# Performance work log

Measured on AMD Instinct MI355X. Metric: run time of the kernel, lower is better.

## Reference

```python
import jax, jax.numpy as jnp
import numpy as np

B, T, D, H = 4, 2048, 1024, 16
HD = D // H  # head_dim = 64

def setup_inputs() -> dict:
    key = jax.random.key(0)
    k1, k2, k3 = jax.random.split(key, 3)
    x = jax.random.normal(k1, (B, T, D), dtype=jnp.float32)
    w_qkv = jax.random.normal(k2, (D, 3 * D), dtype=jnp.float32) * (D ** -0.5)
    b_qkv = jnp.zeros((3 * D,), dtype=jnp.float32)
    w_proj = jax.random.normal(k3, (D, D), dtype=jnp.float32) * (D ** -0.5)
    b_proj = jnp.zeros((D,), dtype=jnp.float32)
    return {"x": x, "w_qkv": w_qkv, "b_qkv": b_qkv, "w_proj": w_proj, "b_proj": b_proj}

def reference(x, w_qkv, b_qkv, w_proj, b_proj):
    b, t, d = x.shape
    scale = HD ** -0.5
    qkv = x @ w_qkv + b_qkv                          # [B,T,3D]
    qkv = qkv.reshape(b, t, 3, H, HD)
    qkv = jnp.transpose(qkv, (2, 0, 3, 1, 4))        # [3,B,H,T,HD]
    q, k, v = qkv[0], qkv[1], qkv[2]
    att = jnp.einsum("bhqd,bhkd->bhqk", q, k) * scale  # [B,H,T,T]
    mask = jnp.tril(jnp.ones((t, t), dtype=att.dtype))[None, None]
    att = att * mask + (1.0 - mask) * (-1e9)
    att = jax.nn.softmax(att, axis=-1)
    # dropout inactive (training=False)
    y = jnp.einsum("bhqk,bhkd->bhqd", att, v)        # [B,H,T,HD]
    y = jnp.transpose(y, (0, 2, 1, 3)).reshape(b, t, d)
    return y @ w_proj + b_proj
```

## Files before the change

kernel.cpp:

```cpp
#include <hip/hip_runtime.h>
#include <hip/hip_bf16.h>

typedef unsigned short u16;
typedef short short8 __attribute__((ext_vector_type(8)));
typedef short bf16x4 __attribute__((ext_vector_type(4)));
typedef float f32x4 __attribute__((ext_vector_type(4)));
typedef float f32x16 __attribute__((ext_vector_type(16)));

#define B_SZ 4
#define T_SEQ 2048
#define DMODEL 1024
#define NH 16
#define HD 64
#define QKV_ELEMS 8388608ull
#define QSCALE (0.125f * 1.44269504f)

__device__ __forceinline__ u16 f2bf(float f) {
    __hip_bfloat16 h = __float2bfloat16(f);
    return __builtin_bit_cast(u16, h);
}

__device__ __forceinline__ void gload16(const void* g, void* l) {
    __builtin_amdgcn_global_load_lds(
        (const __attribute__((address_space(1))) unsigned int*)g,
        (__attribute__((address_space(3))) unsigned int*)l, 16, 0, 0);
}

#define NCX 2048
__global__ __launch_bounds__(256) void prep_kernel(
    const float4* __restrict__ x, u16* __restrict__ xb,
    const float* __restrict__ w_qkv, u16* __restrict__ wqT,
    const float* __restrict__ w_proj, u16* __restrict__ wpT)
{
    const int b = blockIdx.x;
    if (b < NCX) {
        int i = b * 256 + threadIdx.x;
#pragma unroll
        for (int rep = 0; rep < 4; ++rep, i += NCX * 256) {
            const float4 v = x[i];
            union { u16 u[4]; uint2 d; } p;
            p.u[0] = f2bf(v.x); p.u[1] = f2bf(v.y);
            p.u[2] = f2bf(v.z); p.u[3] = f2bf(v.w);
            *(uint2*)(xb + (size_t)i * 4) = p.d;
        }
    } else if (b < NCX + 192) {
        const int bb2 = b - NCX;
        const int n = (bb2 % 12) * 256 + threadIdx.x;
        const int k0 = (bb2 / 12) * 64;
        for (int kk = 0; kk < 64; kk += 8) {
            short8 o;
#pragma unroll
            for (int e = 0; e < 8; ++e)
                o[e] = (short)f2bf(w_qkv[(size_t)(k0 + kk + e) * 3072 + n]);
            *(short8*)&wqT[(size_t)n * 1024 + k0 + kk] = o;
        }
    } else {
        const int bb2 = b - NCX - 192;
        const int n = (bb2 % 4) * 256 + threadIdx.x;
        const int k0 = (bb2 / 4) * 64;
        for (int kk = 0; kk < 64; kk += 8) {
            short8 o;
#pragma unroll
            for (int e = 0; e < 8; ++e)
                o[e] = (short)f2bf(w_proj[(size_t)(k0 + kk + e) * 1024 + n]);
            *(short8*)&wpT[(size_t)n * 1024 + k0 + kk] = o;
        }
    }
}

template <int EPI>
__global__ __launch_bounds__(256) void gemm_kernel(
    const u16* __restrict__ A, const u16* __restrict__ Bt,
    const float* __restrict__ bias, void* __restrict__ outp)
{
    __shared__ u16 As[128 * 64];
    __shared__ u16 Bs[128 * 64];
    const int tid = threadIdx.x;
    const int l = tid & 63;
    const int w = tid >> 6;
    const int wm = w >> 1, wn = w & 1;
    const int m0 = blockIdx.y * 128, n0 = blockIdx.x * 128;
    const int srow = l >> 3;
    const int sch  = (l & 7) ^ srow;
    const int fr = l & 15, fq = l >> 4;

    f32x4 acc[4][4] = {};

    for (int k0 = 0; k0 < 1024; k0 += 64) {
        __syncthreads();
#pragma unroll
        for (int ii = 0; ii < 4; ++ii) {
            const int row = w * 32 + ii * 8;
            gload16(&A[(size_t)(m0 + row + srow) * 1024 + k0 + sch * 8], &As[row * 64]);
            gload16(&Bt[(size_t)(n0 + row + srow) * 1024 + k0 + sch * 8], &Bs[row * 64]);
        }
        __syncthreads();
#pragma unroll
        for (int ks = 0; ks < 2; ++ks) {
            short8 af[4], bf[4];
#pragma unroll
            for (int t = 0; t < 4; ++t) {
                const int ar = wm * 64 + t * 16 + fr;
                af[t] = *(const short8*)&As[ar * 64 + (((ks * 4 + fq) ^ (l & 7)) << 3)];
                const int br = wn * 64 + t * 16 + fr;
                bf[t] = *(const short8*)&Bs[br * 64 + (((ks * 4 + fq) ^ (l & 7)) << 3)];
            }
#pragma unroll
            for (int mt = 0; mt < 4; ++mt)
#pragma unroll
                for (int nt = 0; nt < 4; ++nt)
                    acc[mt][nt] = __builtin_amdgcn_mfma_f32_16x16x32_bf16(
                        af[mt], bf[nt], acc[mt][nt], 0, 0, 0);
        }
    }

    if (EPI == 0) {
        u16* qkv = (u16*)outp;
#pragma unroll
        for (int nt = 0; nt < 4; ++nt) {
            const int n = n0 + wn * 64 + nt * 16 + fr;
            const float bs = bias[n];
            const int which = n >> 10, hh = (n >> 6) & 15, d = n & 63;
            if (which == 2) {
                u16* dst = qkv + 2 * QKV_ELEMS;
#pragma unroll
                for (int mt = 0; mt < 4; ++mt) {
                    const int m = m0 + wm * 64 + mt * 16 + fq * 4;
                    const int bb = m >> 11, t = m & 2047;
                    bf16x4 ov;
#pragma unroll
                    for (int r = 0; r < 4; ++r) ov[r] = (short)f2bf(acc[mt][nt][r] + bs);
                    *(bf16x4*)&dst[(((size_t)(bb * NH + hh)) * HD + d) * T_SEQ + t] = ov;
                }
            } else {
                const float scl = (which == 0) ? QSCALE : 1.0f;
                u16* dst = qkv + (size_t)which * QKV_ELEMS + (size_t)hh * T_SEQ * HD + d;
#pragma unroll
                for (int mt = 0; mt < 4; ++mt)
#pragma unroll
                    for (int r = 0; r < 4; ++r) {
                        const int m = m0 + wm * 64 + mt * 16 + fq * 4 + r;
                        const int bb = m >> 11, t = m & 2047;
                        dst[(size_t)bb * (NH * T_SEQ * HD) + (size_t)t * HD] =
                            f2bf((acc[mt][nt][r] + bs) * scl);
                    }
            }
        }
    } else {
        float* C = (float*)outp;
#pragma unroll
        for (int nt = 0; nt < 4; ++nt) {
            const int n = n0 + wn * 64 + nt * 16 + fr;
            const float bs = bias[n];
#pragma unroll
            for (int mt = 0; mt < 4; ++mt)
#pragma unroll
                for (int r = 0; r < 4; ++r) {
                    const int m = m0 + wm * 64 + mt * 16 + fq * 4 + r;
                    C[(size_t)m * DMODEL + n] = acc[mt][nt][r] + bs;
                }
        }
    }
}

__global__ __launch_bounds__(256) void attn_kernel(
    const u16* __restrict__ q, const u16* __restrict__ k,
    const u16* __restrict__ vT, u16* __restrict__ y)
{
    __shared__ u16 Ks[2][64 * 64];
    __shared__ u16 Vs[2][64 * 64];

    int flat = blockIdx.x;
    flat = (flat & 7) * 64 + (flat >> 3);
    const int qip = flat & 7;
    const int hh = (flat >> 3) & 15;
    const int bb = flat >> 7;

    const size_t hbase = ((size_t)(bb * NH + hh)) * T_SEQ * HD;
    const u16* qb = q + hbase;
    const u16* kb = k + hbase;
    const u16* vTb = vT + hbase;

    const int tid = threadIdx.x;
    const int l = tid & 63;
    const int w = tid >> 6;
    const int qn = l & 31;
    const int h = l >> 5;
    const int srow = l >> 3;
    const int sch = (l & 7) ^ srow;

    u16* Qstage = &Ks[0][0];

    for (int pp = 0; pp < 2; ++pp) {
        const int qi = pp ? (15 - qip) : qip;
        const int q0 = qi * 128;

        __syncthreads();

#pragma unroll
        for (int ii = 0; ii < 4; ++ii) {
            const int row = w * 32 + ii * 8;
            gload16(&qb[(size_t)(q0 + row + srow) * HD + sch * 8], &Qstage[row * 64]);
        }
        {
            const int row = w * 16, row2 = w * 16 + 8;
            gload16(&vTb[(size_t)(row + srow) * T_SEQ + sch * 8], &Vs[0][row * 64]);
            gload16(&vTb[(size_t)(row2 + srow) * T_SEQ + sch * 8], &Vs[0][row2 * 64]);
        }
        __syncthreads();

        short8 qf[4];
        {
            const int qrow = w * 32 + qn;
#pragma unroll
            for (int k16 = 0; k16 < 4; ++k16)
                qf[k16] = *(const short8*)
                    &Qstage[qrow * 64 + (((k16 * 2 + h) ^ (qrow & 7)) << 3)];
        }
        __syncthreads();

        {
            const int row = w * 16, row2 = w * 16 + 8;
            gload16(&kb[(size_t)(row + srow) * HD + sch * 8], &Ks[0][row * 64]);
            gload16(&kb[(size_t)(row2 + srow) * HD + sch * 8], &Ks[0][row2 * 64]);
        }

        const int q0w = q0 + w * 32;
        float l_run = 0.f;
        f32x16 o_acc[2] = {};

        const int nkt = 2 * (qi + 1);
        for (int kt = 0; kt < nkt; ++kt) {
            __syncthreads();
            if (kt + 1 < nkt) {
                const int nb = (kt + 1) & 1;
                const int jj = (kt + 1) * 64;
                const int row = w * 16, row2 = w * 16 + 8;
                gload16(&kb[(size_t)(jj + row + srow) * HD + sch * 8],
                        &Ks[nb][row * 64]);
                gload16(&kb[(size_t)(jj + row2 + srow) * HD + sch * 8],
                        &Ks[nb][row2 * 64]);
                gload16(&vTb[(size_t)(row + srow) * T_SEQ + jj + sch * 8],
                        &Vs[nb][row * 64]);
                gload16(&vTb[(size_t)(row2 + srow) * T_SEQ + jj + sch * 8],
                        &Vs[nb][row2 * 64]);
            }
            const int buf = kt & 1;
            const int j0 = kt * 64;

            if (j0 > q0w + 31) continue;
            const int njt = (j0 + 32 <= q0w + 31) ? 2 : 1;

            f32x16 st[2];
            __builtin_amdgcn_s_setprio(1);
#pragma unroll
            for (int jt = 0; jt < 2; ++jt) {
                if (jt >= njt) continue;
                f32x16 s;
#pragma unroll
                for (int r = 0; r < 16; ++r) s[r] = -16.f;
#pragma unroll
                for (int k16 = 0; k16 < 4; ++k16) {
                    const int jrow = jt * 32 + qn;
                    const short8 kf = *(const short8*)
                        &Ks[buf][jrow * 64 + (((k16 * 2 + h) ^ (jrow & 7)) << 3)];
                    s = __builtin_amdgcn_mfma_f32_32x32x16_bf16(kf, qf[k16], s, 0, 0, 0);
                }
                st[jt] = s;
            }
            __builtin_amdgcn_s_setprio(0);

            const int qg = q0w + qn;
#pragma unroll
            for (int jt = 0; jt < 2; ++jt) {
                if (jt >= njt) continue;
                const bool needMask = (j0 + jt * 32 + 31) > q0w;
                if (needMask) {
#pragma unroll
                    for (int r = 0; r < 16; ++r) {
                        const int jg = j0 + jt * 32 + (r & 3) + 8 * (r >> 2) + 4 * h;
                        if (jg > qg) st[jt][r] = -1e30f;
                    }
                }
            }

            float ls = 0.f;
#pragma unroll
            for (int jt = 0; jt < 2; ++jt) {
                if (jt >= njt) continue;
                float s0 = 0.f, s1 = 0.f, s2 = 0.f, s3 = 0.f;
#pragma unroll
                for (int r = 0; r < 16; r += 4) {
                    float p0 = exp2f(st[jt][r]);
                    float p1 = exp2f(st[jt][r + 1]);
                    float p2 = exp2f(st[jt][r + 2]);
                    float p3 = exp2f(st[jt][r + 3]);
                    st[jt][r] = p0; st[jt][r + 1] = p1;
                    st[jt][r + 2] = p2; st[jt][r + 3] = p3;
                    s0 += p0; s1 += p1; s2 += p2; s3 += p3;
                }
                ls += (s0 + s1) + (s2 + s3);
            }
            ls += __shfl_xor(ls, 32);
            l_run += ls;

            __builtin_amdgcn_s_setprio(1);
#pragma unroll
            for (int jt = 0; jt < 2; ++jt) {
                if (jt >= njt) continue;
#pragma unroll
                for (int g = 0; g < 4; ++g) {
                    bf16x4 pk;
#pragma unroll
                    for (int e = 0; e < 4; ++e) pk[e] = (short)f2bf(st[jt][g * 4 + e]);
#pragma unroll
                    for (int dt = 0; dt < 2; ++dt) {
                        const int drow = dt * 32 + qn;
                        const bf16x4 vf = *(const bf16x4*)
                            &Vs[buf][drow * 64 +
                                     (((jt * 4 + g) ^ (drow & 7)) << 3) + h * 4];
                        o_acc[dt] = __builtin_amdgcn_mfma_f32_32x32x8bf16_1k(
                            vf, pk, o_acc[dt], 0, 0, 0);
                    }
                }
            }
            __builtin_amdgcn_s_setprio(0);
        }

        const float inv = 1.f / l_run;
        const int t = q0 + w * 32 + qn;
        u16* yrow = y + ((size_t)(bb * T_SEQ + t)) * DMODEL + hh * HD;
#pragma unroll
        for (int dt = 0; dt < 2; ++dt)
#pragma unroll
            for (int g = 0; g < 4; ++g) {
                bf16x4 ov;
#pragma unroll
                for (int e = 0; e < 4; ++e)
                    ov[e] = (short)f2bf(o_acc[dt][g * 4 + e] * inv);
                *(bf16x4*)&yrow[dt * 32 + g * 8 + h * 4] = ov;
            }
    }
}

extern "C" void kernel_launch(void* const* d_in, const int* in_sizes, int n_in,
                              void* d_out, int out_size, void* d_ws, size_t ws_size,
                              hipStream_t stream) {
    const float* x      = (const float*)d_in[0];
    const float* w_qkv  = (const float*)d_in[1];
    const float* b_qkv  = (const float*)d_in[2];
    const float* w_proj = (const float*)d_in[3];
    const float* b_proj = (const float*)d_in[4];
    float* out = (float*)d_out;

    u16* xb  = (u16*)d_ws;
    u16* wqT = xb + 8388608;
    u16* wpT = wqT + 3145728;
    u16* qkv = wpT + 1048576;
    u16* yb  = qkv + 3 * QKV_ELEMS;

    prep_kernel<<<2304, 256, 0, stream>>>((const float4*)x, xb,
                                          w_qkv, wqT, w_proj, wpT);
    gemm_kernel<0><<<dim3(24, 64), 256, 0, stream>>>(xb, wqT, b_qkv, (void*)qkv);
    attn_kernel<<<dim3(512), 256, 0, stream>>>(
        qkv, qkv + QKV_ELEMS, qkv + 2 * QKV_ELEMS, yb);
    gemm_kernel<1><<<dim3(8, 64), 256, 0, stream>>>(yb, wpT, b_proj, (void*)out);
}
```

Baseline: 285.1 us.

## Split attention key tiles across two wave groups with LDS reduction

The attention kernel now launches 512 threads per block. Two groups of four waves each take one 32-key half of every 64-key tile, and the two partial outputs and row sums are merged through shared memory at the end. Each wave does half the QK/PV MFMA work per tile, which should give more parallelism and latency hiding per block. The cost is an extra reduction pass through LDS plus barriers, and half the waves sit idle during the final normalise-and-store. Register pressure and occupancy also change under launch_bounds(512,4).

```diff
diff --git a/kernel.cpp b/kernel.cpp
--- a/kernel.cpp
+++ b/kernel.cpp
@@ -163,12 +163,13 @@
     }
 }
 
-__global__ __launch_bounds__(256) void attn_kernel(
+__global__ __launch_bounds__(512, 4) void attn_kernel(
     const u16* __restrict__ q, const u16* __restrict__ k,
     const u16* __restrict__ vT, u16* __restrict__ y)
 {
     __shared__ u16 Ks[2][64 * 64];
     __shared__ u16 Vs[2][64 * 64];
+    __shared__ float Lx[256];
 
     int flat = blockIdx.x;
     flat = (flat & 7) * 64 + (flat >> 3);
@@ -183,7 +184,9 @@
 
     const int tid = threadIdx.x;
     const int l = tid & 63;
-    const int w = tid >> 6;
+    const int wid = tid >> 6;
+    const int w4 = wid & 3;
+    const int jtw = wid >> 2;
     const int qn = l & 31;
     const int h = l >> 5;
     const int srow = l >> 3;
@@ -197,21 +200,20 @@
 
         __syncthreads();
 
-#pragma unroll
-        for (int ii = 0; ii < 4; ++ii) {
-            const int row = w * 32 + ii * 8;
+        {
+            const int row = wid * 16, row2 = wid * 16 + 8;
             gload16(&qb[(size_t)(q0 + row + srow) * HD + sch * 8], &Qstage[row * 64]);
+            gload16(&qb[(size_t)(q0 + row2 + srow) * HD + sch * 8], &Qstage[row2 * 64]);
         }
         {
-            const int row = w * 16, row2 = w * 16 + 8;
+            const int row = wid * 8;
             gload16(&vTb[(size_t)(row + srow) * T_SEQ + sch * 8], &Vs[0][row * 64]);
-            gload16(&vTb[(size_t)(row2 + srow) * T_SEQ + sch * 8], &Vs[0][row2 * 64]);
         }
         __syncthreads();
 
         short8 qf[4];
         {
-            const int qrow = w * 32 + qn;
+            const int qrow = w4 * 32 + qn;
 #pragma unroll
             for (int k16 = 0; k16 < 4; ++k16)
                 qf[k16] = *(const short8*)
@@ -220,12 +222,11 @@
         __syncthreads();
 
         {
-            const int row = w * 16, row2 = w * 16 + 8;
+            const int row = wid * 8;
             gload16(&kb[(size_t)(row + srow) * HD + sch * 8], &Ks[0][row * 64]);
-            gload16(&kb[(size_t)(row2 + srow) * HD + sch * 8], &Ks[0][row2 * 64]);
-        }
-
-        const int q0w = q0 + w * 32;
+        }
+
+        const int q0w = q0 + w4 * 32;
         float l_run = 0.f;
         f32x16 o_acc[2] = {};
 
@@ -235,111 +236,122 @@
             if (kt + 1 < nkt) {
                 const int nb = (kt + 1) & 1;
                 const int jj = (kt + 1) * 64;
-                const int row = w * 16, row2 = w * 16 + 8;
+                const int row = wid * 8;
                 gload16(&kb[(size_t)(jj + row + srow) * HD + sch * 8],
                         &Ks[nb][row * 64]);
-                gload16(&kb[(size_t)(jj + row2 + srow) * HD + sch * 8],
-                        &Ks[nb][row2 * 64]);
                 gload16(&vTb[(size_t)(row + srow) * T_SEQ + jj + sch * 8],
                         &Vs[nb][row * 64]);
-                gload16(&vTb[(size_t)(row2 + srow) * T_SEQ + jj + sch * 8],
-                        &Vs[nb][row2 * 64]);
             }
             const int buf = kt & 1;
-            const int j0 = kt * 64;
-
-            if (j0 > q0w + 31) continue;
-            const int njt = (j0 + 32 <= q0w + 31) ? 2 : 1;
-
-            f32x16 st[2];
+            const int jb = kt * 64 + jtw * 32;
+
+            if (jb > q0w + 31) continue;
+
+            f32x16 st;
             __builtin_amdgcn_s_setprio(1);
-#pragma unroll
-            for (int jt = 0; jt < 2; ++jt) {
-                if (jt >= njt) continue;
+            {
                 f32x16 s;
 #pragma unroll
                 for (int r = 0; r < 16; ++r) s[r] = -16.f;
 #pragma unroll
                 for (int k16 = 0; k16 < 4; ++k16) {
-                    const int jrow = jt * 32 + qn;
+                    const int jrow = jtw * 32 + qn;
                     const short8 kf = *(const short8*)
                         &Ks[buf][jrow * 64 + (((k16 * 2 + h) ^ (jrow & 7)) << 3)];
                     s = __builtin_amdgcn_mfma_f32_32x32x16_bf16(kf, qf[k16], s, 0, 0, 0);
                 }
-                st[jt] = s;
+                st = s;
             }
             __builtin_amdgcn_s_setprio(0);
 
             const int qg = q0w + qn;
-#pragma unroll
-            for (int jt = 0; jt < 2; ++jt) {
-                if (jt >= njt) continue;
-                const bool needMask = (j0 + jt * 32 + 31) > q0w;
-                if (needMask) {
-#pragma unroll
-                    for (int r = 0; r < 16; ++r) {
-                        const int jg = j0 + jt * 32 + (r & 3) + 8 * (r >> 2) + 4 * h;
-                        if (jg > qg) st[jt][r] = -1e30f;
-                    }
-                }
-            }
-
-            float ls = 0.f;
-#pragma unroll
-            for (int jt = 0; jt < 2; ++jt) {
-                if (jt >= njt) continue;
-                float s0 = 0.f, s1 = 0.f, s2 = 0.f, s3 = 0.f;
-#pragma unroll
-                for (int r = 0; r < 16; r += 4) {
-                    float p0 = exp2f(st[jt][r]);
-                    float p1 = exp2f(st[jt][r + 1]);
-                    float p2 = exp2f(st[jt][r + 2]);
-                    float p3 = exp2f(st[jt][r + 3]);
-                    st[jt][r] = p0; st[jt][r + 1] = p1;
-                    st[jt][r + 2] = p2; st[jt][r + 3] = p3;
-                    s0 += p0; s1 += p1; s2 += p2; s3 += p3;
-                }
-                ls += (s0 + s1) + (s2 + s3);
-            }
+            if (jb + 31 > q0w) {
+#pragma unroll
+                for (int r = 0; r < 16; ++r) {
+                    const int jg = jb + (r & 3) + 8 * (r >> 2) + 4 * h;
+                    if (jg > qg) st[r] = -1e30f;
+                }
+            }
+
+            float s0 = 0.f, s1 = 0.f, s2 = 0.f, s3 = 0.f;
+#pragma unroll
+            for (int r = 0; r < 16; r += 4) {
+                float p0 = exp2f(st[r]);
+                float p1 = exp2f(st[r + 1]);
+                float p2 = exp2f(st[r + 2]);
+                float p3 = exp2f(st[r + 3]);
+                st[r] = p0; st[r + 1] = p1; st[r + 2] = p2; st[r + 3] = p3;
+                s0 += p0; s1 += p1; s2 += p2; s3 += p3;
+            }
+            float ls = (s0 + s1) + (s2 + s3);
             ls += __shfl_xor(ls, 32);
             l_run += ls;
 
             __builtin_amdgcn_s_setprio(1);
 #pragma unroll
-            for (int jt = 0; jt < 2; ++jt) {
-                if (jt >= njt) continue;
+            for (int g = 0; g < 4; ++g) {
+                bf16x4 pk;
+#pragma unroll
+                for (int e = 0; e < 4; ++e) pk[e] = (short)f2bf(st[g * 4 + e]);
+#pragma unroll
+                for (int dt = 0; dt < 2; ++dt) {
+                    const int drow = dt * 32 + qn;
+                    const bf16x4 vf = *(const bf16x4*)
+                        &Vs[buf][drow * 64 +
+                                 (((jtw * 4 + g) ^ (drow & 7)) << 3) + h * 4];
+                    o_acc[dt] = __builtin_amdgcn_mfma_f32_32x32x8bf16_1k(
+                        vf, pk, o_acc[dt], 0, 0, 0);
+                }
+            }
+            __builtin_amdgcn_s_setprio(0);
+        }
+
+        __syncthreads();
+        const int ridx = w4 * 64 + l;
+        if (jtw == 1) {
+#pragma unroll
+            for (int dt = 0; dt < 2; ++dt) {
+                float* xo = dt ? (float*)&Vs[0][0] : (float*)&Ks[0][0];
 #pragma unroll
                 for (int g = 0; g < 4; ++g) {
-                    bf16x4 pk;
-#pragma unroll
-                    for (int e = 0; e < 4; ++e) pk[e] = (short)f2bf(st[jt][g * 4 + e]);
-#pragma unroll
-                    for (int dt = 0; dt < 2; ++dt) {
-                        const int drow = dt * 32 + qn;
-                        const bf16x4 vf = *(const bf16x4*)
-                            &Vs[buf][drow * 64 +
-                                     (((jt * 4 + g) ^ (drow & 7)) << 3) + h * 4];
-                        o_acc[dt] = __builtin_amdgcn_mfma_f32_32x32x8bf16_1k(
-                            vf, pk, o_acc[dt], 0, 0, 0);
-                    }
-                }
-            }
-            __builtin_amdgcn_s_setprio(0);
-        }
-
-        const float inv = 1.f / l_run;
-        const int t = q0 + w * 32 + qn;
-        u16* yrow = y + ((size_t)(bb * T_SEQ + t)) * DMODEL + hh * HD;
-#pragma unroll
-        for (int dt = 0; dt < 2; ++dt)
-#pragma unroll
-            for (int g = 0; g < 4; ++g) {
-                bf16x4 ov;
-#pragma unroll
-                for (int e = 0; e < 4; ++e)
-                    ov[e] = (short)f2bf(o_acc[dt][g * 4 + e] * inv);
-                *(bf16x4*)&yrow[dt * 32 + g * 8 + h * 4] = ov;
-            }
+                    f32x4 v;
+#pragma unroll
+                    for (int e = 0; e < 4; ++e) v[e] = o_acc[dt][g * 4 + e];
+                    *(f32x4*)&xo[ridx * 16 + ((g ^ (ridx & 3)) << 2)] = v;
+                }
+            }
+            Lx[ridx] = l_run;
+        }
+        __syncthreads();
+        if (jtw == 0) {
+#pragma unroll
+            for (int dt = 0; dt < 2; ++dt) {
+                const float* xo = dt ? (const float*)&Vs[0][0]
+                                     : (const float*)&Ks[0][0];
+#pragma unroll
+                for (int g = 0; g < 4; ++g) {
+                    const f32x4 v =
+                        *(const f32x4*)&xo[ridx * 16 + ((g ^ (ridx & 3)) << 2)];
+#pragma unroll
+                    for (int e = 0; e < 4; ++e) o_acc[dt][g * 4 + e] += v[e];
+                }
+            }
+            const float lt = l_run + Lx[ridx];
+
+            const float inv = 1.f / lt;
+            const int t = q0 + w4 * 32 + qn;
+            u16* yrow = y + ((size_t)(bb * T_SEQ + t)) * DMODEL + hh * HD;
+#pragma unroll
+            for (int dt = 0; dt < 2; ++dt)
+#pragma unroll
+                for (int g = 0; g < 4; ++g) {
+                    bf16x4 ov;
+#pragma unroll
+                    for (int e = 0; e < 4; ++e)
+                        ov[e] = (short)f2bf(o_acc[dt][g * 4 + e] * inv);
+                    *(bf16x4*)&yrow[dt * 32 + g * 8 + h * 4] = ov;
+                }
+        }
     }
 }
 
@@ -362,7 +374,7 @@
     prep_kernel<<<2304, 256, 0, stream>>>((const float4*)x, xb,
                                           w_qkv, wqT, w_proj, wpT);
     gemm_kernel<0><<<dim3(24, 64), 256, 0, stream>>>(xb, wqT, b_qkv, (void*)qkv);
-    attn_kernel<<<dim3(512), 256, 0, stream>>>(
+    attn_kernel<<<dim3(512), 512, 0, stream>>>(
         qkv, qkv + QKV_ELEMS, qkv + 2 * QKV_ELEMS, yb);
     gemm_kernel<1><<<dim3(8, 64), 256, 0, stream>>>(yb, wpT, b_proj, (void*)out);
 }
```

After: 272.3 us. -4.5%, faster.
